# Optimization experiments

Measured on AMD Instinct MI355X. Metric: run time of the kernel, lower is better.

The kernel has to match this reference:

```python
import jax, jax.numpy as jnp
import numpy as np
import math

DISTANCE_TAU = 1.0
MAX_DISTANCE = 5


def _diamond_offsets(max_distance):
    """List of (weight, dx, dy) for all offsets with |dx|+|dy| == d, d in 1..max_distance."""
    offs = []
    for d in range(1, max_distance + 1):
        w = math.exp(-d / DISTANCE_TAU)
        for dx in range(-d, d + 1):
            rem = d - abs(dx)
            for dy in sorted({rem, -rem}):
                offs.append((w, dx, dy))
    return offs


def setup_inputs() -> dict:
    key = jax.random.key(0)
    B, H, W = 64, 1024, 1024
    grid_spikes = jax.random.normal(key, (B, H, W), dtype=jnp.float32)
    return {"grid_spikes": grid_spikes}


def reference(grid_spikes) -> jnp.ndarray:
    # I_internal = sum_d w_d * sum_{|dx|+|dy|=d} roll(roll(s, dx, H-axis), dy, W-axis)
    out = jnp.zeros_like(grid_spikes)
    for w, dx, dy in _diamond_offsets(MAX_DISTANCE):
        out = out + jnp.asarray(w, grid_spikes.dtype) * jnp.roll(grid_spikes, (dx, dy), axis=(1, 2))
    return out
```

## Files before the change

### kernel.cpp

```cpp
#include <hip/hip_runtime.h>

#define HH 1024
#define WW 1024
#define BM 32
#define BN 256
#define RPT 8
#define WAVES 4
#define TROWS (BM + 10)
#define TCOLS 272
#define TFLOATS (TROWS * TCOLS)
#define NSTG ((TFLOATS + 255) / 256)
#define LDSF (NSTG * 256)
#define NXCD 8
#define GX (WW / BN)
#define GY (HH / BM)

typedef __attribute__((address_space(1))) const float gfloat;
typedef __attribute__((address_space(3))) float sfloat;
typedef float vfloat4 __attribute__((ext_vector_type(4)));

__global__ __launch_bounds__(256) void diamond_kernel(const float* __restrict__ in,
                                                      float* __restrict__ out,
                                                      int nblocks) {
    __shared__ __attribute__((aligned(16))) float tile[LDSF];

    const int wgid = blockIdx.x;
    const int k0   = (wgid % NXCD) * (nblocks / NXCD) + wgid / NXCD;
    const int b    = k0 / (GX * GY);
    const int rem  = k0 % (GX * GY);
    const int gy   = rem / GX;
    const int gx   = rem % GX;

    const int tj  = threadIdx.x;
    const int ty  = threadIdx.y;
    const int J0  = gx * BN;
    const int i0b = gy * BM;
    const float* __restrict__ src = in  + (size_t)b * HH * WW;
    float*       __restrict__ dst = out + (size_t)b * HH * WW;

#pragma unroll
    for (int n = 0; n < 12; ++n) {
        const int I = ty + 4 * n;
        if (I < NSTG) {
            const int f = I * 256 + 4 * tj;
            const int r = f / TCOLS;
            const int c = f - r * TCOLS;
            const int gr = (i0b + r - 5) & (HH - 1);
            const int gc = (J0 - 8 + c) & (WW - 1);
            __builtin_amdgcn_global_load_lds((gfloat*)(src + (size_t)gr * WW + gc),
                                             (sfloat*)&tile[I * 256], 16, 0, 0);
        }
    }
    __syncthreads();

    const float EV[6] = {1.0f,
                         0.36787944117144233f,
                         0.1353352832366127f,
                         0.049787068367863944f,
                         0.018315638888734179f,
                         0.006737946999085467f};

    float acc[RPT][4];
#pragma unroll
    for (int m = 0; m < RPT; ++m)
#pragma unroll
        for (int p = 0; p < 4; ++p) acc[m][p] = 0.0f;

    const int base_r = ty * RPT;

#pragma unroll
    for (int rr = 0; rr < RPT + 10; ++rr) {
        const float* trow = &tile[(base_r + rr) * TCOLS + 4 * tj];

        const int gr = (i0b + base_r + rr - 5) & (HH - 1);
        const float4 own =
            *reinterpret_cast<const float4*>(src + (size_t)gr * WW + J0 + 4 * tj);

        float s[20];
        {
            float4 v0 = *reinterpret_cast<const float4*>(trow + 0);
            float4 v1 = *reinterpret_cast<const float4*>(trow + 4);
            float4 v3 = *reinterpret_cast<const float4*>(trow + 12);
            float4 v4 = *reinterpret_cast<const float4*>(trow + 16);
            s[0]  = v0.x; s[1]  = v0.y; s[2]  = v0.z; s[3]  = v0.w;
            s[4]  = v1.x; s[5]  = v1.y; s[6]  = v1.z; s[7]  = v1.w;
            s[8]  = own.x; s[9] = own.y; s[10] = own.z; s[11] = own.w;
            s[12] = v3.x; s[13] = v3.y; s[14] = v3.z; s[15] = v3.w;
            s[16] = v4.x; s[17] = v4.y; s[18] = v4.z; s[19] = v4.w;
        }

        float Hc[4];
#pragma unroll
        for (int p = 0; p < 4; ++p) Hc[p] = s[8 + p];
        {
            const int m1 = rr - 10, m2 = rr;
            if (m1 >= 0 && m1 < RPT)
#pragma unroll
                for (int p = 0; p < 4; ++p) acc[m1][p] = fmaf(EV[5], Hc[p], acc[m1][p]);
            if (m2 >= 0 && m2 < RPT)
#pragma unroll
                for (int p = 0; p < 4; ++p) acc[m2][p] = fmaf(EV[5], Hc[p], acc[m2][p]);
        }
#pragma unroll
        for (int k = 1; k <= 4; ++k) {
#pragma unroll
            for (int p = 0; p < 4; ++p)
                Hc[p] = fmaf(EV[k], s[8 + p - k] + s[8 + p + k], Hc[p]);
            const int a = 5 - k;
            const int m1 = rr - 10 + k, m2 = rr - k;
            if (m1 >= 0 && m1 < RPT)
#pragma unroll
                for (int p = 0; p < 4; ++p) acc[m1][p] = fmaf(EV[a], Hc[p], acc[m1][p]);
            if (m2 >= 0 && m2 < RPT && m2 != m1)
#pragma unroll
                for (int p = 0; p < 4; ++p) acc[m2][p] = fmaf(EV[a], Hc[p], acc[m2][p]);
        }
        {
#pragma unroll
            for (int p = 0; p < 4; ++p)
                Hc[p] = fmaf(EV[5], s[8 + p - 5] + s[8 + p + 5], Hc[p]);
            const int m = rr - 5;
            if (m >= 0 && m < RPT)
#pragma unroll
                for (int p = 0; p < 4; ++p) acc[m][p] += Hc[p] - s[8 + p];
        }
    }

#pragma unroll
    for (int m = 0; m < RPT; ++m) {
        vfloat4 v = {acc[m][0], acc[m][1], acc[m][2], acc[m][3]};
        __builtin_nontemporal_store(
            v, reinterpret_cast<vfloat4*>(dst + (size_t)(i0b + base_r + m) * WW + J0 + 4 * tj));
    }
}

extern "C" void kernel_launch(void* const* d_in, const int* in_sizes, int n_in,
                              void* d_out, int out_size, void* d_ws, size_t ws_size,
                              hipStream_t stream) {
    const float* in  = (const float*)d_in[0];
    float*       out = (float*)d_out;
    const int B = in_sizes[0] / (HH * WW);
    const int nblocks = GX * GY * B;
    dim3 block(64, WAVES, 1);
    dim3 grid(nblocks, 1, 1);
    hipLaunchKernelGGL(diamond_kernel, grid, block, 0, stream, in, out, nblocks);
}
```

Before: 96.61 us.

## Use single-wave workgroups with per-wave LDS halo tiles and no barrier

Shrinks each workgroup to one wavefront handling 8 output rows, with its own 18-row LDS tile. The workgroup barrier is replaced by a vmcnt wait. This removes inter-wave synchronization and lets waves proceed independently. In exchange the vertical halo overhead rises, so more redundant global loads go into LDS per output row.

After: 128.0 us. 32.5% more time.

```diff
diff --git a/kernel.cpp b/kernel.cpp
--- a/kernel.cpp
+++ b/kernel.cpp
@@ -2,26 +2,22 @@
 
 #define HH 1024
 #define WW 1024
-#define BM 32
-#define BN 256
 #define RPT 8
-#define WAVES 4
-#define TROWS (BM + 10)
+#define NR (RPT + 10)
 #define TCOLS 272
-#define TFLOATS (TROWS * TCOLS)
-#define NSTG ((TFLOATS + 255) / 256)
+#define NSTG 20
 #define LDSF (NSTG * 256)
 #define NXCD 8
-#define GX (WW / BN)
-#define GY (HH / BM)
+#define GX (WW / 256)
+#define GY (HH / RPT)
 
 typedef __attribute__((address_space(1))) const float gfloat;
 typedef __attribute__((address_space(3))) float sfloat;
 typedef float vfloat4 __attribute__((ext_vector_type(4)));
 
-__global__ __launch_bounds__(256) void diamond_kernel(const float* __restrict__ in,
-                                                      float* __restrict__ out,
-                                                      int nblocks) {
+__global__ __launch_bounds__(64) void diamond_kernel(const float* __restrict__ in,
+                                                     float* __restrict__ out,
+                                                     int nblocks) {
     __shared__ __attribute__((aligned(16))) float tile[LDSF];
 
     const int wgid = blockIdx.x;
@@ -32,26 +28,23 @@
     const int gx   = rem % GX;
 
     const int tj  = threadIdx.x;
-    const int ty  = threadIdx.y;
-    const int J0  = gx * BN;
-    const int i0b = gy * BM;
+    const int J0  = gx * 256;
+    const int i0  = gy * RPT;
     const float* __restrict__ src = in  + (size_t)b * HH * WW;
     float*       __restrict__ dst = out + (size_t)b * HH * WW;
 
 #pragma unroll
-    for (int n = 0; n < 12; ++n) {
-        const int I = ty + 4 * n;
-        if (I < NSTG) {
-            const int f = I * 256 + 4 * tj;
-            const int r = f / TCOLS;
-            const int c = f - r * TCOLS;
-            const int gr = (i0b + r - 5) & (HH - 1);
-            const int gc = (J0 - 8 + c) & (WW - 1);
-            __builtin_amdgcn_global_load_lds((gfloat*)(src + (size_t)gr * WW + gc),
-                                             (sfloat*)&tile[I * 256], 16, 0, 0);
-        }
+    for (int I = 0; I < NSTG; ++I) {
+        const int f = I * 256 + 4 * tj;
+        const int r = f / TCOLS;
+        const int c = f - r * TCOLS;
+        const int gr = (i0 + r - 5) & (HH - 1);
+        const int gc = (J0 - 8 + c) & (WW - 1);
+        __builtin_amdgcn_global_load_lds((gfloat*)(src + (size_t)gr * WW + gc),
+                                         (sfloat*)&tile[I * 256], 16, 0, 0);
     }
-    __syncthreads();
+    asm volatile("s_waitcnt vmcnt(0)" ::: "memory");
+    __builtin_amdgcn_sched_barrier(0);
 
     const float EV[6] = {1.0f,
                          0.36787944117144233f,
@@ -66,28 +59,24 @@
 #pragma unroll
         for (int p = 0; p < 4; ++p) acc[m][p] = 0.0f;
 
-    const int base_r = ty * RPT;
+#pragma unroll
+    for (int rr = 0; rr < NR; ++rr) {
+        const int gr = (i0 + rr - 5) & (HH - 1);
+        const float* trow = &tile[rr * TCOLS + 4 * tj];
 
-#pragma unroll
-    for (int rr = 0; rr < RPT + 10; ++rr) {
-        const float* trow = &tile[(base_r + rr) * TCOLS + 4 * tj];
-
-        const int gr = (i0b + base_r + rr - 5) & (HH - 1);
         const float4 own =
             *reinterpret_cast<const float4*>(src + (size_t)gr * WW + J0 + 4 * tj);
+        float4 v0 = *reinterpret_cast<const float4*>(trow + 0);
+        float4 v1 = *reinterpret_cast<const float4*>(trow + 4);
+        float4 v3 = *reinterpret_cast<const float4*>(trow + 12);
+        float4 v4 = *reinterpret_cast<const float4*>(trow + 16);
 
         float s[20];
-        {
-            float4 v0 = *reinterpret_cast<const float4*>(trow + 0);
-            float4 v1 = *reinterpret_cast<const float4*>(trow + 4);
-            float4 v3 = *reinterpret_cast<const float4*>(trow + 12);
-            float4 v4 = *reinterpret_cast<const float4*>(trow + 16);
-            s[0]  = v0.x; s[1]  = v0.y; s[2]  = v0.z; s[3]  = v0.w;
-            s[4]  = v1.x; s[5]  = v1.y; s[6]  = v1.z; s[7]  = v1.w;
-            s[8]  = own.x; s[9] = own.y; s[10] = own.z; s[11] = own.w;
-            s[12] = v3.x; s[13] = v3.y; s[14] = v3.z; s[15] = v3.w;
-            s[16] = v4.x; s[17] = v4.y; s[18] = v4.z; s[19] = v4.w;
-        }
+        s[0]  = v0.x; s[1]  = v0.y; s[2]  = v0.z; s[3]  = v0.w;
+        s[4]  = v1.x; s[5]  = v1.y; s[6]  = v1.z; s[7]  = v1.w;
+        s[8]  = own.x; s[9] = own.y; s[10] = own.z; s[11] = own.w;
+        s[12] = v3.x; s[13] = v3.y; s[14] = v3.z; s[15] = v3.w;
+        s[16] = v4.x; s[17] = v4.y; s[18] = v4.z; s[19] = v4.w;
 
         float Hc[4];
 #pragma unroll
@@ -130,7 +119,7 @@
     for (int m = 0; m < RPT; ++m) {
         vfloat4 v = {acc[m][0], acc[m][1], acc[m][2], acc[m][3]};
         __builtin_nontemporal_store(
-            v, reinterpret_cast<vfloat4*>(dst + (size_t)(i0b + base_r + m) * WW + J0 + 4 * tj));
+            v, reinterpret_cast<vfloat4*>(dst + (size_t)(i0 + m) * WW + J0 + 4 * tj));
     }
 }
 
@@ -141,7 +130,7 @@
     float*       out = (float*)d_out;
     const int B = in_sizes[0] / (HH * WW);
     const int nblocks = GX * GY * B;
-    dim3 block(64, WAVES, 1);
+    dim3 block(64, 1, 1);
     dim3 grid(nblocks, 1, 1);
     hipLaunchKernelGGL(diamond_kernel, grid, block, 0, stream, in, out, nblocks);
 }
```
